# Kernel optimization log

Hardware: AMD Instinct MI355X
Metric: run time of the kernel (lower is better)

## Reference

```python
import jax, jax.numpy as jnp
import numpy as np

B, F0, D = 2048, 39, 16
LAYER_SIZES = [128, 128, 128]  # split_half=True -> field_nums [39, 64, 64]


def setup_inputs() -> dict:
    key = jax.random.key(0)
    ks = jax.random.split(key, 1 + 2 * len(LAYER_SIZES))
    inputs = jax.random.normal(ks[0], (B, F0, D), dtype=jnp.float32)
    out = {"inputs": inputs}
    field_nums = [F0]
    for i, size in enumerate(LAYER_SIZES):
        fk = field_nums[-1]
        fan_in = F0 * fk  # conv1d filter fan-in (kernel width 1)
        scale = np.sqrt(2.0 / (fan_in + size)).astype(np.float32)  # glorot
        # filter stored as [F0, Fk, size]; TF flat index is h0*Fk + hk
        out[f"w{i}"] = jax.random.normal(ks[1 + 2 * i], (F0, fk, size), dtype=jnp.float32) * scale
        out[f"b{i}"] = jnp.zeros((size,), dtype=jnp.float32)
        field_nums.append(size // 2)  # split_half=True
    return out


def reference(inputs, w0, w1, w2, b0, b1, b2):
    # CIN: per-embedding-dim outer product of x0 and x_{k-1}, then 1x1 conv
    # (shared dense over field pairs). Fused here as a single einsum per layer.
    x0 = inputs  # [B, F0, D]
    xk = inputs  # [B, Fk, D]
    params = [(w0, b0), (w1, b1), (w2, b2)]
    n_layers = len(params)
    direct = []
    for idx, (W, b) in enumerate(params):
        # out[b, s, d] = sum_{h,k} x0[b,h,d] * xk[b,k,d] * W[h,k,s]
        z = jnp.einsum('bhd,bkd,hks->bsd', x0, xk, W) + b[None, :, None]
        z = jax.nn.relu(z)  # activation='relu'
        if idx != n_layers - 1:
            half = z.shape[1] // 2  # split_half: first half feeds next layer
            xk = z[:, :half, :]
            direct.append(z[:, half:, :])
        else:
            direct.append(z)
    logit = jnp.sum(jnp.concatenate(direct, axis=1), axis=-1)  # [B, 64+64+128]
    return logit
```

## Files before the change

kernel.cpp:

```cpp
#include <hip/hip_runtime.h>
#include <stdint.h>
#include <stddef.h>

#define F0N  39
#define SN   128
#define NB   8
#define X0TS 44
#define XKTS 72
#define WBLK 8192
#define NHB2 234

typedef __attribute__((ext_vector_type(8))) short short8;
typedef __attribute__((ext_vector_type(4))) float floatx4;

__device__ __forceinline__ uint16_t f2bf(float f) {
  uint32_t u = __float_as_uint(f);
  u += 0x7fffu + ((u >> 16) & 1u);
  return (uint16_t)(u >> 16);
}

__global__ __launch_bounds__(256) void cin_prepass(
    const float* __restrict__ w0, const float* __restrict__ w1,
    const float* __restrict__ w2, uint16_t* __restrict__ wt) {
  __shared__ float T[32 * 132];
  const int bc = blockIdx.x;
  const int ch = bc & 1;
  const int lh = bc >> 1;
  const int L = lh / F0N;
  const int h = lh - L * F0N;
  const float* W = (L == 0) ? w0 : ((L == 1) ? w1 : w2);
  const int fk = (L == 0) ? 39 : 64;
  const int tid = threadIdx.x;

  for (int e = tid; e < 4096; e += 256) {
    int kc = e >> 7, s = e & 127;
    int k = ch * 32 + kc;
    T[kc * 132 + s] = (k < fk) ? W[(h * fk + k) * SN + s] : 0.0f;
  }
  __syncthreads();
  uint32_t* dst = (uint32_t*)(wt + (size_t)lh * WBLK);
  for (int i = tid; i < 2048; i += 256) {
    int st = i >> 8, w = i & 255;
    int ln = w >> 2, jp = w & 3;
    int quad = ln >> 4, l16 = ln & 15;
    int k0 = quad * 8 + jp * 2;
    int s = st * 16 + l16;
    dst[(size_t)(st * 2 + ch) * 256 + w] =
        (uint32_t)f2bf(T[k0 * 132 + s]) | ((uint32_t)f2bf(T[(k0 + 1) * 132 + s]) << 16);
  }
}

__global__ __launch_bounds__(1024) void cin_main(
    const float* __restrict__ x,
    const float* __restrict__ bias0, const float* __restrict__ bias1,
    const float* __restrict__ bias2,
    const uint16_t* __restrict__ wt,
    float* __restrict__ out) {

  __shared__ __align__(16) float    X0T[NB * 16 * X0TS];
  __shared__ __align__(16) uint16_t XKT[NB * 16 * XKTS];

  const int tid  = threadIdx.x;
  const int lane = tid & 63;
  const int wave = tid >> 6;
  const int st   = wave >> 1;
  const int bg   = wave & 1;
  const int l16  = lane & 15;
  const int quad = lane >> 4;
  const int bbase = blockIdx.x * NB;

  {
    float* p = X0T;
#pragma unroll
    for (int i = 0; i < 6; i++) { int e = tid + 1024 * i; if (e < 5632) p[e] = 0.f; }
    uint32_t* q = (uint32_t*)XKT;
#pragma unroll
    for (int i = 0; i < 5; i++) { int e = tid + 1024 * i; if (e < 4608) q[e] = 0u; }
  }
  __syncthreads();

#pragma unroll
  for (int it = 0; it < 5; ++it) {
    int e = tid + it * 1024;
    if (e < NB * F0N * 16) {
      float v = x[(size_t)bbase * (F0N * 16) + e];
      int d = e & 15, p = e >> 4;
      int b = p / F0N, h = p - b * F0N;
      X0T[(b * 16 + d) * X0TS + h] = v;
    }
  }
  __syncthreads();

  if (tid < 512) {
    int b = tid >> 6, d = (tid >> 2) & 15, kg = tid & 3;
    const float* src = &X0T[(b * 16 + d) * X0TS];
    uint32_t* drow = (uint32_t*)&XKT[(b * 16 + d) * XKTS + kg * 16];
#pragma unroll
    for (int i2 = 0; i2 < 8; i2++) {
      int k0 = kg * 16 + i2 * 2;
      uint32_t lo = (k0 < 39)     ? (uint32_t)f2bf(src[k0])     : 0u;
      uint32_t hi = (k0 + 1 < 39) ? (uint32_t)f2bf(src[k0 + 1]) : 0u;
      drow[i2] = lo | (hi << 16);
    }
  }
  __syncthreads();

  const uint16_t* wlane = wt + st * 1024 + (size_t)lane * 8;

  short8 Wc0 = *(const short8*)(wlane);
  short8 Wc1 = *(const short8*)(wlane + 512);

#pragma unroll 1
  for (int L = 0; L < 3; ++L) {
    short8 Bf0[4], Bf1[4];
#pragma unroll
    for (int bi = 0; bi < 4; ++bi) {
      const uint16_t* r = XKT + ((bg * 4 + bi) * 16 + l16) * XKTS + quad * 8;
      Bf0[bi] = *(const short8*)r;
      Bf1[bi] = *(const short8*)(r + 32);
    }
    const float* bp = (L == 0) ? bias0 : ((L == 1) ? bias1 : bias2);
    float bvr[4];
#pragma unroll
    for (int r = 0; r < 4; ++r) bvr[r] = bp[st * 16 + quad * 4 + r];

    floatx4 z[4] = {};
    const floatx4 zero4 = {0.f, 0.f, 0.f, 0.f};

#pragma unroll 1
    for (int h = 0; h < 40; ++h) {
      short8 Wn0, Wn1;
      {
        int Ln = L, hh = h + 1;
        if (hh >= 39) { if (L < 2) { Ln = L + 1; hh = 0; } else hh = 38; }
        const uint16_t* wl = wlane + (size_t)(Ln * F0N + hh) * WBLK;
        Wn0 = *(const short8*)wl;
        Wn1 = *(const short8*)(wl + 512);
      }

      float xs[4];
#pragma unroll
      for (int bi = 0; bi < 4; ++bi)
        xs[bi] = X0T[((bg * 4 + bi) * 16 + l16) * X0TS + h];

#pragma unroll
      for (int bi = 0; bi < 4; ++bi) {
        floatx4 y = __builtin_amdgcn_mfma_f32_16x16x32_bf16(Wc0, Bf0[bi], zero4, 0, 0, 0);
        y = __builtin_amdgcn_mfma_f32_16x16x32_bf16(Wc1, Bf1[bi], y, 0, 0, 0);
#pragma unroll
        for (int r = 0; r < 4; ++r) z[bi][r] += xs[bi] * y[r];
      }
      Wc0 = Wn0;
      Wc1 = Wn1;
    }

#pragma unroll
    for (int bi = 0; bi < 4; ++bi) {
      const int b = bg * 4 + bi;
#pragma unroll
      for (int r = 0; r < 4; ++r) {
        float t = fmaxf(z[bi][r] + bvr[r], 0.f);
        if (L < 2 && st < 4)
          XKT[(b * 16 + l16) * XKTS + st * 16 + quad * 4 + r] = f2bf(t);
        float s4 = t;
        s4 += __shfl_xor(s4, 1);
        s4 += __shfl_xor(s4, 2);
        s4 += __shfl_xor(s4, 4);
        s4 += __shfl_xor(s4, 8);
        if (l16 == 0) {
          int s = st * 16 + quad * 4 + r;
          if (L == 2)       out[(size_t)(bbase + b) * 256 + 128 + s] = s4;
          else if (s >= 64) out[(size_t)(bbase + b) * 256 + L * 64 + (s - 64)] = s4;
        }
      }
    }
    if (L < 2) __syncthreads();
  }
}

extern "C" void kernel_launch(void* const* d_in, const int* in_sizes, int n_in,
                              void* d_out, int out_size, void* d_ws, size_t ws_size,
                              hipStream_t stream) {
  (void)in_sizes; (void)n_in; (void)out_size; (void)ws_size;
  const float* x  = (const float*)d_in[0];
  const float* w0 = (const float*)d_in[1];
  const float* b0 = (const float*)d_in[2];
  const float* w1 = (const float*)d_in[3];
  const float* b1 = (const float*)d_in[4];
  const float* w2 = (const float*)d_in[5];
  const float* b2 = (const float*)d_in[6];
  uint16_t* wt    = (uint16_t*)d_ws;

  cin_prepass<<<NHB2, 256, 0, stream>>>(w0, w1, w2, wt);
  cin_main<<<256, 1024, 0, stream>>>(x, b0, b1, b2, wt, (float*)d_out);
}
```

Baseline: 135.4 us.

## Prefetch weight fragments two steps ahead and pad X0T stride

Deepens the software pipeline for bf16 weight fragment loads from one step to two, using a flattened global step index across layers. It also prefetches the next x0 scalars from shared memory one iteration ahead. The X0T row stride changes from 44 to 45 floats to avoid LDS bank conflicts on the strided per-lane reads. The cost is extra registers for the additional prefetch buffers, which may reduce occupancy at 1024 threads.

Measured after the change: 146.2 us. 8.0% more time.

```diff
diff --git a/kernel.cpp b/kernel.cpp
--- a/kernel.cpp
+++ b/kernel.cpp
@@ -5,7 +5,7 @@
 #define F0N  39
 #define SN   128
 #define NB   8
-#define X0TS 44
+#define X0TS 45
 #define XKTS 72
 #define WBLK 8192
 #define NHB2 234
@@ -57,7 +57,7 @@
     const uint16_t* __restrict__ wt,
     float* __restrict__ out) {
 
-  __shared__ __align__(16) float    X0T[NB * 16 * X0TS];
+  __shared__ float    X0T[NB * 16 * X0TS];
   __shared__ __align__(16) uint16_t XKT[NB * 16 * XKTS];
 
   const int tid  = threadIdx.x;
@@ -72,7 +72,7 @@
   {
     float* p = X0T;
 #pragma unroll
-    for (int i = 0; i < 6; i++) { int e = tid + 1024 * i; if (e < 5632) p[e] = 0.f; }
+    for (int i = 0; i < 6; i++) { int e = tid + 1024 * i; if (e < 5760) p[e] = 0.f; }
     uint32_t* q = (uint32_t*)XKT;
 #pragma unroll
     for (int i = 0; i < 5; i++) { int e = tid + 1024 * i; if (e < 4608) q[e] = 0u; }
@@ -107,8 +107,17 @@
 
   const uint16_t* wlane = wt + st * 1024 + (size_t)lane * 8;
 
-  short8 Wc0 = *(const short8*)(wlane);
-  short8 Wc1 = *(const short8*)(wlane + 512);
+  auto wstep = [&](int g) -> const uint16_t* {
+    int Lp = (g * 205) >> 13;
+    int hp = g - Lp * 40;
+    if (hp > 38) hp = 38;
+    return wlane + (size_t)(Lp * F0N + hp) * WBLK;
+  };
+
+  short8 Wc0 = *(const short8*)wstep(0);
+  short8 Wc1 = *(const short8*)(wstep(0) + 512);
+  short8 Wn0 = *(const short8*)wstep(1);
+  short8 Wn1 = *(const short8*)(wstep(1) + 512);
 
 #pragma unroll 1
   for (int L = 0; L < 3; ++L) {
@@ -127,31 +136,37 @@
     floatx4 z[4] = {};
     const floatx4 zero4 = {0.f, 0.f, 0.f, 0.f};
 
+    float xsC[4];
+#pragma unroll
+    for (int bi = 0; bi < 4; ++bi)
+      xsC[bi] = X0T[((bg * 4 + bi) * 16 + l16) * X0TS + 0];
+
 #pragma unroll 1
     for (int h = 0; h < 40; ++h) {
-      short8 Wn0, Wn1;
+      short8 W20, W21;
       {
-        int Ln = L, hh = h + 1;
-        if (hh >= 39) { if (L < 2) { Ln = L + 1; hh = 0; } else hh = 38; }
-        const uint16_t* wl = wlane + (size_t)(Ln * F0N + hh) * WBLK;
-        Wn0 = *(const short8*)wl;
-        Wn1 = *(const short8*)(wl + 512);
+        int gp = L * 40 + h + 2;
+        if (gp > 119) gp = 119;
+        const uint16_t* wl = wstep(gp);
+        W20 = *(const short8*)wl;
+        W21 = *(const short8*)(wl + 512);
       }
-
-      float xs[4];
+      float xsN[4];
 #pragma unroll
       for (int bi = 0; bi < 4; ++bi)
-        xs[bi] = X0T[((bg * 4 + bi) * 16 + l16) * X0TS + h];
+        xsN[bi] = X0T[((bg * 4 + bi) * 16 + l16) * X0TS + h + 1];
 
 #pragma unroll
       for (int bi = 0; bi < 4; ++bi) {
         floatx4 y = __builtin_amdgcn_mfma_f32_16x16x32_bf16(Wc0, Bf0[bi], zero4, 0, 0, 0);
         y = __builtin_amdgcn_mfma_f32_16x16x32_bf16(Wc1, Bf1[bi], y, 0, 0, 0);
 #pragma unroll
-        for (int r = 0; r < 4; ++r) z[bi][r] += xs[bi] * y[r];
+        for (int r = 0; r < 4; ++r) z[bi][r] += xsC[bi] * y[r];
       }
-      Wc0 = Wn0;
-      Wc1 = Wn1;
+      Wc0 = Wn0; Wc1 = Wn1;
+      Wn0 = W20; Wn1 = W21;
+#pragma unroll
+      for (int bi = 0; bi < 4; ++bi) xsC[bi] = xsN[bi];
     }
 
 #pragma unroll
```
